# Optimization experiments

Hardware: AMD Instinct MI355X
Metric: run time of the kernel (lower is better)

The kernel has to match this reference:

```python
import jax, jax.numpy as jnp
import numpy as np

N_NODES, D, B, NEG2, DRUG_NUM = 20000, 512, 2048, 64, 2000
H1, H2 = 128, 64


def setup_inputs() -> dict:
    ks = jax.random.split(jax.random.key(0), 10)
    embed = jax.random.normal(ks[0], (N_NODES, D), dtype=jnp.float32)
    h = jax.random.randint(ks[1], (B, 1), 0, DRUG_NUM)
    t = jax.random.randint(ks[2], (B, 1), 0, N_NODES)
    n_s = jax.random.randint(ks[3], (B, NEG2), 0, DRUG_NUM)  # all < drug_num -> chunk branch
    s1 = 1.0 / np.sqrt(2 * D)
    s2 = 1.0 / np.sqrt(H1)
    s3 = 1.0 / np.sqrt(H2)
    W1 = jax.random.uniform(ks[4], (2 * D, H1), minval=-s1, maxval=s1, dtype=jnp.float32)
    b1 = jax.random.uniform(ks[5], (H1,), minval=-s1, maxval=s1, dtype=jnp.float32)
    W2 = jax.random.uniform(ks[6], (H1, H2), minval=-s2, maxval=s2, dtype=jnp.float32)
    b2 = jax.random.uniform(ks[7], (H2,), minval=-s2, maxval=s2, dtype=jnp.float32)
    W3 = jax.random.uniform(ks[8], (H2, 1), minval=-s3, maxval=s3, dtype=jnp.float32)
    b3 = jax.random.uniform(ks[9], (1,), minval=-s3, maxval=s3, dtype=jnp.float32)
    return {"embed": embed, "W1": W1, "b1": b1, "W2": W2, "b2": b2, "W3": W3, "b3": b3,
            "h": h, "t": t, "n_s": n_s}


def _mlp(x, W1, b1, W2, b2, W3, b3):
    # [..., 2D] -> [...] score
    x = jax.nn.relu(x @ W1 + b1)
    x = jax.nn.relu(x @ W2 + b2)
    return (x @ W3 + b3)[..., 0]


def reference(embed, W1, b1, W2, b2, W3, b3, h, t, n_s):
    K = n_s.shape[1] // 2
    n_t, n_h = n_s[:, :K], n_s[:, K:]
    h_e = embed[h]          # [B, 1, D]
    t_e = embed[t]          # [B, T, D]
    T = t.shape[1]
    # positive pairs: [B, T]
    pos = _mlp(jnp.concatenate([jnp.tile(h_e, (1, T, 1)), t_e], axis=-1),
               W1, b1, W2, b2, W3, b3)
    # corrupted-tail negatives: [B, K]
    neg1 = _mlp(jnp.concatenate([jnp.tile(h_e, (1, K, 1)), embed[n_t]], axis=-1),
                W1, b1, W2, b2, W3, b3)
    # corrupted-head negatives: [B, T*K] (T=1 here)
    neg2 = _mlp(jnp.concatenate([embed[n_h], jnp.tile(t_e, (1, K, 1))], axis=-1),
                W1, b1, W2, b2, W3, b3)
    neg = jnp.concatenate([neg1, neg2], axis=1)  # [B, 2K]
    return pos, neg
```

## Files before the change

### kernel.cpp

```cpp
#include <hip/hip_runtime.h>

#define DIM    512
#define BATCH  2048
#define NDRUG  2000
#define H1     128
#define H2     64
#define NITEM  65
#define SLAB   774144
#define W2F_OFF  (SLAB)
#define W1F_OFF  (W2F_OFF + 4096)
#define X1_OFF   (W1F_OFF + 65536)
#define X2_OFF   (X1_OFF + 512000)

typedef __attribute__((ext_vector_type(8))) short short8;
typedef __attribute__((ext_vector_type(4))) float floatx4;

__device__ inline unsigned f2bf(float x) {
    union { float f; unsigned u; } v; v.f = x;
    unsigned r = v.u + 0x7fffu + ((v.u >> 16) & 1u);
    return r >> 16;
}

__device__ inline unsigned pkbf(float a, float b) {
    return f2bf(a) | (f2bf(b) << 16);
}

__device__ inline short8 cvt8(const float* __restrict__ src) {
    float4 a = *(const float4*)src, b = *(const float4*)(src + 4);
    union { short8 s; unsigned u[4]; } v;
    v.u[0] = pkbf(a.x, a.y); v.u[1] = pkbf(a.z, a.w);
    v.u[2] = pkbf(b.x, b.y); v.u[3] = pkbf(b.z, b.w);
    return v.s;
}

__global__ __launch_bounds__(256) void prep(
    const float* __restrict__ embed, const float* __restrict__ W1,
    const float* __restrict__ W2, const int* __restrict__ t,
    float* __restrict__ ws)
{
    const int blk = blockIdx.x, tid = threadIdx.x;
    if (blk < 125) {
        short8* X1 = (short8*)(ws + X1_OFF);
        #pragma unroll
        for (int i = 0; i < 4; ++i) {
            int u = blk * 1024 + i * 256 + tid;
            int row = u >> 6, c = u & 63;
            X1[u] = cvt8(embed + (size_t)row * DIM + c * 8);
        }
    } else if (blk < 253) {
        short8* X2 = (short8*)(ws + X2_OFF);
        #pragma unroll
        for (int i = 0; i < 4; ++i) {
            int u = (blk - 125) * 1024 + i * 256 + tid;
            int row = u >> 6, c = u & 63;
            X2[u] = cvt8(embed + (size_t)t[row] * DIM + c * 8);
        }
    } else if (blk < 317) {
        short8* W1f = (short8*)(ws + W1F_OFF);
        int item = (blk - 253) * 256 + tid;
        int frag = item >> 6, lane = item & 63;
        int half = frag >> 7, kt = (frag >> 3) & 15, nt = frag & 7;
        int n = lane & 15, q = lane >> 4;
        short8 v;
        #pragma unroll
        for (int j = 0; j < 8; ++j) {
            int k = half * DIM + kt * 32 + q * 8 + j;
            v[j] = (short)f2bf(W1[k * H1 + nt * 16 + n]);
        }
        W1f[item] = v;
    } else {
        short8* W2f = (short8*)(ws + W2F_OFF);
        #pragma unroll
        for (int i = 0; i < 4; ++i) {
            int item = i * 256 + tid;
            int frag = item >> 6, lane = item & 63;
            int kt = frag >> 2, nt = frag & 3;
            int n = lane & 15, q = lane >> 4;
            short8 v;
            #pragma unroll
            for (int j = 0; j < 8; ++j)
                v[j] = (short)f2bf(W2[(kt * 32 + q * 8 + j) * H2 + nt * 16 + n]);
            W2f[item] = v;
        }
    }
}

__global__ __launch_bounds__(256) void layer1_mfma(
    float* __restrict__ ws, const float* __restrict__ b1)
{
    const short8* W1f = (const short8*)(ws + W1F_OFF);
    const int lane = threadIdx.x & 63;
    const int w    = blockIdx.x * 4 + (threadIdx.x >> 6);
    const int n = lane & 15, q = lane >> 4;

    const short8* Xrow;
    float* obase;
    int half, nt;
    bool tail;
    if (w < 2000) {
        int rt = w >> 4, cv = w & 15;
        tail = cv >= 8;
        nt   = cv & 7;
        half = tail ? 1 : 0;
        Xrow = (const short8*)(ws + X1_OFF) + (size_t)(rt * 16 + n) * 64;
        obase = ws + (tail ? NDRUG * H1 : 0) + (size_t)(rt * 16) * H1 + nt * 16;
    } else {
        int w2 = w - 2000;
        int rt = w2 >> 3;
        nt   = w2 & 7;
        half = 1;
        tail = true;
        Xrow = (const short8*)(ws + X2_OFF) + (size_t)(rt * 16 + n) * 64;
        obase = ws + 2 * (NDRUG * H1) + (size_t)(rt * 16) * H1 + nt * 16;
    }

    floatx4 acc0 = (floatx4){0.f, 0.f, 0.f, 0.f};
    floatx4 acc1 = (floatx4){0.f, 0.f, 0.f, 0.f};
    const int fbase = (half * 16) * 8 + nt;
    #pragma unroll
    for (int kt = 0; kt < 16; kt += 2) {
        short8 a0 = Xrow[kt * 4 + q];
        short8 a1 = Xrow[(kt + 1) * 4 + q];
        short8 b0 = W1f[(size_t)(fbase + kt * 8) * 64 + lane];
        short8 b1f = W1f[(size_t)(fbase + (kt + 1) * 8) * 64 + lane];
        acc0 = __builtin_amdgcn_mfma_f32_16x16x32_bf16(a0, b0, acc0, 0, 0, 0);
        acc1 = __builtin_amdgcn_mfma_f32_16x16x32_bf16(a1, b1f, acc1, 0, 0, 0);
    }

    const float badd = tail ? b1[nt * 16 + n] : 0.f;
    #pragma unroll
    for (int reg = 0; reg < 4; ++reg)
        obase[(q * 4 + reg) * H1 + n] = acc0[reg] + acc1[reg] + badd;
}

__global__ __launch_bounds__(256) void score_mfma(
    const float* __restrict__ ws,
    const float* __restrict__ b2, const float* __restrict__ W3,
    const float* __restrict__ b3,
    const int* __restrict__ h, const int* __restrict__ ns,
    float* __restrict__ out)
{
    const float* P  = ws;
    const float* Q  = ws + NDRUG * H1;
    const float* Qt = Q + NDRUG * H1;
    const short8* W2f = (const short8*)(ws + W2F_OFF);

    const int lane = threadIdx.x & 63;
    const int wv   = threadIdx.x >> 6;
    const int tile = blockIdx.x * 4 + wv;
    const int n = lane & 15, q = lane >> 4;

    const int sg   = tile * 16 + n;
    const int b    = sg / NITEM;
    const int item = sg - b * NITEM;
    const float *Pr, *Qr;
    if (item == 0)       { Pr = P + h[b] * H1;                        Qr = Qt + b * H1; }
    else if (item <= 32) { Pr = P + h[b] * H1;                        Qr = Q + ns[b * 64 + item - 1] * H1; }
    else                 { Pr = P + ns[b * 64 + 32 + item - 33] * H1; Qr = Qt + b * H1; }

    floatx4 acc[4];
    #pragma unroll
    for (int nt = 0; nt < 4; ++nt) acc[nt] = (floatx4){0.f, 0.f, 0.f, 0.f};

    #pragma unroll
    for (int kt = 0; kt < 4; ++kt) {
        const int kb = kt * 32 + q * 8;
        float4 p0 = *(const float4*)(Pr + kb);
        float4 p1 = *(const float4*)(Pr + kb + 4);
        float4 q0 = *(const float4*)(Qr + kb);
        float4 q1 = *(const float4*)(Qr + kb + 4);
        union { short8 s; unsigned u[4]; } A;
        A.u[0] = pkbf(fmaxf(p0.x + q0.x, 0.f), fmaxf(p0.y + q0.y, 0.f));
        A.u[1] = pkbf(fmaxf(p0.z + q0.z, 0.f), fmaxf(p0.w + q0.w, 0.f));
        A.u[2] = pkbf(fmaxf(p1.x + q1.x, 0.f), fmaxf(p1.y + q1.y, 0.f));
        A.u[3] = pkbf(fmaxf(p1.z + q1.z, 0.f), fmaxf(p1.w + q1.w, 0.f));
        #pragma unroll
        for (int nt = 0; nt < 4; ++nt) {
            short8 bf = W2f[(kt * 4 + nt) * 64 + lane];
            acc[nt] = __builtin_amdgcn_mfma_f32_16x16x32_bf16(A.s, bf, acc[nt], 0, 0, 0);
        }
    }

    float part[4];
    #pragma unroll
    for (int reg = 0; reg < 4; ++reg) {
        float sum = 0.f;
        #pragma unroll
        for (int nt = 0; nt < 4; ++nt) {
            int j = nt * 16 + n;
            sum = fmaf(fmaxf(acc[nt][reg] + b2[j], 0.f), W3[j], sum);
        }
        part[reg] = sum;
    }
    #pragma unroll
    for (int m = 1; m < 16; m <<= 1) {
        #pragma unroll
        for (int reg = 0; reg < 4; ++reg)
            part[reg] += __shfl_xor(part[reg], m, 64);
    }
    if (n == 0) {
        const float base3 = b3[0];
        #pragma unroll
        for (int reg = 0; reg < 4; ++reg) {
            int gid = tile * 16 + q * 4 + reg;
            int bb  = gid / NITEM;
            int it  = gid - bb * NITEM;
            float val = part[reg] + base3;
            if (it == 0) out[bb] = val;
            else         out[BATCH + bb * 64 + (it - 1)] = val;
        }
    }
}

extern "C" void kernel_launch(void* const* d_in, const int* in_sizes, int n_in,
                              void* d_out, int out_size, void* d_ws, size_t ws_size,
                              hipStream_t stream) {
    const float* embed = (const float*)d_in[0];
    const float* W1    = (const float*)d_in[1];
    const float* b1    = (const float*)d_in[2];
    const float* W2    = (const float*)d_in[3];
    const float* b2    = (const float*)d_in[4];
    const float* W3    = (const float*)d_in[5];
    const float* b3    = (const float*)d_in[6];
    const int*   h     = (const int*)d_in[7];
    const int*   t     = (const int*)d_in[8];
    const int*   ns    = (const int*)d_in[9];
    float* out = (float*)d_out;
    float* ws  = (float*)d_ws;

    prep<<<318, 256, 0, stream>>>(embed, W1, W2, t, ws);
    layer1_mfma<<<756, 256, 0, stream>>>(ws, b1);
    score_mfma<<<(BATCH * NITEM) / 64, 256, 0, stream>>>(ws, b2, W3, b3,
                                                         h, ns, out);
}
```

Measured before the change: 120.2 us.

## Fuse embedding bf16 conversion into layer1 via LDS-staged row tiles

Removes the separate conversion pass that wrote bf16 copies of the embedding rows (X1, X2) to the workspace. Instead, each layer1 block converts its 16 embedding rows into padded LDS and reuses them across four waves, each computing several output column tiles. This avoids a workspace write and read-back round trip and cuts block count. The cost is fewer blocks (253) and more work per wave, which may reduce parallelism and latency hiding.

After: 117.5 us. -2.2%, faster.

```diff
diff --git a/kernel.cpp b/kernel.cpp
--- a/kernel.cpp
+++ b/kernel.cpp
@@ -9,8 +9,7 @@
 #define SLAB   774144
 #define W2F_OFF  (SLAB)
 #define W1F_OFF  (W2F_OFF + 4096)
-#define X1_OFF   (W1F_OFF + 65536)
-#define X2_OFF   (X1_OFF + 512000)
+#define LP       65
 
 typedef __attribute__((ext_vector_type(8))) short short8;
 typedef __attribute__((ext_vector_type(4))) float floatx4;
@@ -20,11 +19,9 @@
     unsigned r = v.u + 0x7fffu + ((v.u >> 16) & 1u);
     return r >> 16;
 }
-
 __device__ inline unsigned pkbf(float a, float b) {
     return f2bf(a) | (f2bf(b) << 16);
 }
-
 __device__ inline short8 cvt8(const float* __restrict__ src) {
     float4 a = *(const float4*)src, b = *(const float4*)(src + 4);
     union { short8 s; unsigned u[4]; } v;
@@ -33,31 +30,14 @@
     return v.s;
 }
 
-__global__ __launch_bounds__(256) void prep(
-    const float* __restrict__ embed, const float* __restrict__ W1,
-    const float* __restrict__ W2, const int* __restrict__ t,
+__global__ __launch_bounds__(256) void pack_w(
+    const float* __restrict__ W1, const float* __restrict__ W2,
     float* __restrict__ ws)
 {
     const int blk = blockIdx.x, tid = threadIdx.x;
-    if (blk < 125) {
-        short8* X1 = (short8*)(ws + X1_OFF);
-        #pragma unroll
-        for (int i = 0; i < 4; ++i) {
-            int u = blk * 1024 + i * 256 + tid;
-            int row = u >> 6, c = u & 63;
-            X1[u] = cvt8(embed + (size_t)row * DIM + c * 8);
-        }
-    } else if (blk < 253) {
-        short8* X2 = (short8*)(ws + X2_OFF);
-        #pragma unroll
-        for (int i = 0; i < 4; ++i) {
-            int u = (blk - 125) * 1024 + i * 256 + tid;
-            int row = u >> 6, c = u & 63;
-            X2[u] = cvt8(embed + (size_t)t[row] * DIM + c * 8);
-        }
-    } else if (blk < 317) {
+    if (blk < 64) {
         short8* W1f = (short8*)(ws + W1F_OFF);
-        int item = (blk - 253) * 256 + tid;
+        int item = blk * 256 + tid;
         int frag = item >> 6, lane = item & 63;
         int half = frag >> 7, kt = (frag >> 3) & 15, nt = frag & 7;
         int n = lane & 15, q = lane >> 4;
@@ -85,52 +65,80 @@
     }
 }
 
-__global__ __launch_bounds__(256) void layer1_mfma(
-    float* __restrict__ ws, const float* __restrict__ b1)
+__global__ __launch_bounds__(256) void layer1(
+    const float* __restrict__ embed, const float* __restrict__ b1,
+    const int* __restrict__ t, float* __restrict__ ws)
 {
+    __shared__ short8 ldsA[16 * LP];
     const short8* W1f = (const short8*)(ws + W1F_OFF);
-    const int lane = threadIdx.x & 63;
-    const int w    = blockIdx.x * 4 + (threadIdx.x >> 6);
+    const int blk = blockIdx.x, tid = threadIdx.x;
+    const bool isPQ = blk < 125;
+    const int rowbase = isPQ ? blk * 16 : (blk - 125) * 16;
+
+    #pragma unroll
+    for (int i = 0; i < 4; ++i) {
+        int u = i * 256 + tid;
+        int r = u >> 6, c = u & 63;
+        size_t grow = isPQ ? (size_t)(rowbase + r) : (size_t)t[rowbase + r];
+        ldsA[r * LP + c] = cvt8(embed + grow * DIM + c * 8);
+    }
+    __syncthreads();
+
+    const int lane = tid & 63, wv = tid >> 6;
     const int n = lane & 15, q = lane >> 4;
 
-    const short8* Xrow;
-    float* obase;
-    int half, nt;
-    bool tail;
-    if (w < 2000) {
-        int rt = w >> 4, cv = w & 15;
-        tail = cv >= 8;
-        nt   = cv & 7;
-        half = tail ? 1 : 0;
-        Xrow = (const short8*)(ws + X1_OFF) + (size_t)(rt * 16 + n) * 64;
-        obase = ws + (tail ? NDRUG * H1 : 0) + (size_t)(rt * 16) * H1 + nt * 16;
+    if (isPQ) {
+        const int T0 = wv * 4;
+        const int half = (T0 >= 8) ? 1 : 0;
+        floatx4 acc[4];
+        #pragma unroll
+        for (int i = 0; i < 4; ++i) acc[i] = (floatx4){0.f, 0.f, 0.f, 0.f};
+        #pragma unroll
+        for (int kt = 0; kt < 16; ++kt) {
+            short8 a = ldsA[n * LP + kt * 4 + q];
+            #pragma unroll
+            for (int i = 0; i < 4; ++i) {
+                int nt = (T0 + i) & 7;
+                short8 bf = W1f[(size_t)(((half * 16 + kt) * 8) + nt) * 64 + lane];
+                acc[i] = __builtin_amdgcn_mfma_f32_16x16x32_bf16(a, bf, acc[i], 0, 0, 0);
+            }
+        }
+        float* tbl = ws + (half ? NDRUG * H1 : 0);
+        #pragma unroll
+        for (int i = 0; i < 4; ++i) {
+            int nt = (T0 + i) & 7;
+            float badd = half ? b1[nt * 16 + n] : 0.f;
+            #pragma unroll
+            for (int reg = 0; reg < 4; ++reg)
+                tbl[(size_t)(rowbase + q * 4 + reg) * H1 + nt * 16 + n] =
+                    acc[i][reg] + badd;
+        }
     } else {
-        int w2 = w - 2000;
-        int rt = w2 >> 3;
-        nt   = w2 & 7;
-        half = 1;
-        tail = true;
-        Xrow = (const short8*)(ws + X2_OFF) + (size_t)(rt * 16 + n) * 64;
-        obase = ws + 2 * (NDRUG * H1) + (size_t)(rt * 16) * H1 + nt * 16;
-    }
-
-    floatx4 acc0 = (floatx4){0.f, 0.f, 0.f, 0.f};
-    floatx4 acc1 = (floatx4){0.f, 0.f, 0.f, 0.f};
-    const int fbase = (half * 16) * 8 + nt;
-    #pragma unroll
-    for (int kt = 0; kt < 16; kt += 2) {
-        short8 a0 = Xrow[kt * 4 + q];
-        short8 a1 = Xrow[(kt + 1) * 4 + q];
-        short8 b0 = W1f[(size_t)(fbase + kt * 8) * 64 + lane];
-        short8 b1f = W1f[(size_t)(fbase + (kt + 1) * 8) * 64 + lane];
-        acc0 = __builtin_amdgcn_mfma_f32_16x16x32_bf16(a0, b0, acc0, 0, 0, 0);
-        acc1 = __builtin_amdgcn_mfma_f32_16x16x32_bf16(a1, b1f, acc1, 0, 0, 0);
-    }
-
-    const float badd = tail ? b1[nt * 16 + n] : 0.f;
-    #pragma unroll
-    for (int reg = 0; reg < 4; ++reg)
-        obase[(q * 4 + reg) * H1 + n] = acc0[reg] + acc1[reg] + badd;
+        const int T0 = wv * 2;
+        floatx4 acc[2];
+        #pragma unroll
+        for (int i = 0; i < 2; ++i) acc[i] = (floatx4){0.f, 0.f, 0.f, 0.f};
+        #pragma unroll
+        for (int kt = 0; kt < 16; ++kt) {
+            short8 a = ldsA[n * LP + kt * 4 + q];
+            #pragma unroll
+            for (int i = 0; i < 2; ++i) {
+                int nt = T0 + i;
+                short8 bf = W1f[(size_t)(((16 + kt) * 8) + nt) * 64 + lane];
+                acc[i] = __builtin_amdgcn_mfma_f32_16x16x32_bf16(a, bf, acc[i], 0, 0, 0);
+            }
+        }
+        float* tbl = ws + 2 * (NDRUG * H1);
+        #pragma unroll
+        for (int i = 0; i < 2; ++i) {
+            int nt = T0 + i;
+            float badd = b1[nt * 16 + n];
+            #pragma unroll
+            for (int reg = 0; reg < 4; ++reg)
+                tbl[(size_t)(rowbase + q * 4 + reg) * H1 + nt * 16 + n] =
+                    acc[i][reg] + badd;
+        }
+    }
 }
 
 __global__ __launch_bounds__(256) void score_mfma(
@@ -228,8 +236,8 @@
     float* out = (float*)d_out;
     float* ws  = (float*)d_ws;
 
-    prep<<<318, 256, 0, stream>>>(embed, W1, W2, t, ws);
-    layer1_mfma<<<756, 256, 0, stream>>>(ws, b1);
+    pack_w<<<65, 256, 0, stream>>>(W1, W2, ws);
+    layer1<<<253, 256, 0, stream>>>(embed, b1, t, ws);
     score_mfma<<<(BATCH * NITEM) / 64, 256, 0, stream>>>(ws, b2, W3, b3,
                                                          h, ns, out);
 }
```
